# Performance work log

Measured on AMD Instinct MI355X. Metric: run time of the kernel, lower is better.

## Reference

```python
import jax, jax.numpy as jnp
import numpy as np

B = 131072
IN_DIM = 310   # 300 + zdimension_Gap(10)
H1 = 128       # g_neural_network_width
D = 100        # hard-coded data_t / generate_data width
SLOPE = 0.01   # torch LeakyReLU default negative_slope


def _leaky(v):
    return jnp.where(v >= 0, v, SLOPE * v)


def setup_inputs() -> dict:
    key = jax.random.key(0)
    ks = jax.random.split(key, 8)
    # kaiming_normal fan_in, a=0: std = sqrt(2 / fan_in)
    W1 = jax.random.normal(ks[0], (IN_DIM, 10), jnp.float32) * np.sqrt(2.0 / IN_DIM)
    b1 = jnp.zeros((10,), jnp.float32)
    W2 = jax.random.normal(ks[1], (10, H1), jnp.float32) * np.sqrt(2.0 / 10)
    b2 = jnp.zeros((H1,), jnp.float32)
    W3 = jax.random.normal(ks[2], (H1, 2), jnp.float32) * np.sqrt(2.0 / H1)
    b3 = jnp.zeros((2,), jnp.float32)
    x = jax.random.normal(ks[3], (B, IN_DIM), jnp.float32)
    data_t = jax.random.normal(ks[4], (B, D), jnp.float32)
    return {"x": x, "data_t": data_t, "W1": W1, "b1": b1,
            "W2": W2, "b2": b2, "W3": W3, "b3": b3}


def reference(x, data_t, W1, b1, W2, b2, W3, b3):
    # 3-layer MLP with LeakyReLU -> coeff [B, 2]
    h = _leaky(x @ W1 + b1)
    h = _leaky(h @ W2 + b2)
    coeff = _leaky(h @ W3 + b3)
    # polynomial basis: only power-1 (data_t) and power-2 (data_t**2) terms are used
    t2 = data_t * data_t  # [B, D]
    # generate_data[i] = coeff[i,0]*data_t[i] + coeff[i,1]*data_t[i]**2 (vectorized over batch)
    generate_data = coeff[:, 0:1] * data_t + coeff[:, 1:2] * t2
    return generate_data
```

## Files before the change

kernel.cpp:

```cpp
#include <hip/hip_runtime.h>
#include <stdint.h>

typedef float f32x2 __attribute__((ext_vector_type(2)));
typedef float f32x4 __attribute__((ext_vector_type(4)));

#define TILE_F 19840
#define NTPB   4
#define PSTR   82
#define CP_OFF 5248
#define CPSTR  18
#define A_F    8192
#define APW    1024
#define BPW    1456
#define LDSF   (TILE_F + 128)
#define LDS_BYTES (LDSF * 4)

__device__ __forceinline__ float leaky(float v) { return fmaxf(v, 0.01f * v); }
__device__ __forceinline__ f32x2 leaky2(f32x2 v) {
    return __builtin_elementwise_max(v, v * 0.01f);
}

__device__ __forceinline__ void gload16(const float* g, float* l) {
    auto gp = reinterpret_cast<const float __attribute__((address_space(1)))*>(
        reinterpret_cast<uintptr_t>(g));
    auto lp = reinterpret_cast<float __attribute__((address_space(3)))*>(
        reinterpret_cast<uintptr_t>(l));
    __builtin_amdgcn_global_load_lds(gp, lp, 16, 0, 0);
}

__device__ __forceinline__ void stage_B(const float* src, float* dst, int lane) {
    #pragma unroll
    for (int i = 0; i < 5; ++i) gload16(src + i * 256, dst + i * 256);
    if (lane < 44) gload16(src + 5 * 256, dst + 5 * 256);
}
__device__ __forceinline__ void stage_A(const float* src, float* dst) {
    #pragma unroll
    for (int i = 0; i < 4; ++i) gload16(src + i * 256, dst + i * 256);
}

template<int KQ>
__device__ __forceinline__ void fma_xk(const float* xk, const float* __restrict__ Wb,
                                       float* acc) {
    #pragma unroll
    for (int k = 0; k < KQ; ++k) {
        #pragma unroll
        for (int j = 0; j < 10; ++j)
            acc[j] = fmaf(xk[k], Wb[k * 10 + j], acc[j]);
    }
}

__global__ __launch_bounds__(512, 4) void gen_mlp_r14(
    const float* __restrict__ x, const float* __restrict__ data_t,
    const float* __restrict__ W1, const float* __restrict__ b1,
    const float* __restrict__ W2, const float* __restrict__ b2,
    const float* __restrict__ W3, const float* __restrict__ b3,
    float* __restrict__ out)
{
    extern __shared__ float lds[];
    float* buf = lds;
    float* ccs = lds + TILE_F;

    const int t    = threadIdx.x;
    const int lane = t & 63;
    const int row  = lane;
    const int wq   = __builtin_amdgcn_readfirstlane(t >> 6);

    const int tile0 = blockIdx.x * NTPB;

    {
        const float* g = x + (size_t)tile0 * TILE_F;
        stage_A(g + wq * APW + lane * 4,       buf + wq * APW);
        stage_B(g + A_F + wq * BPW + lane * 4, buf + A_F + wq * BPW, lane);
    }
    asm volatile("s_waitcnt vmcnt(0)" ::: "memory");
    __builtin_amdgcn_s_barrier();

    #pragma unroll 1
    for (int it = 0; it < NTPB; ++it) {
        const int tile  = tile0 + it;
        const int tnext = (it + 1 < NTPB) ? tile + 1 : tile0;
        const float* gnext = x + (size_t)tnext * TILE_F;

        const f32x4* dt4 = (const f32x4*)data_t + (size_t)tile * 1600;
        f32x4 tv0 = dt4[t], tv1 = dt4[512 + t], tv2 = dt4[1024 + t], tv3;
        if (t < 64) tv3 = dt4[1536 + t];

        float xk[40];
        {
            const float* xr = buf + row * 310 + wq * 40;
            if (wq == 7) {
                #pragma unroll
                for (int q = 0; q < 15; ++q)
                    *(f32x2*)&xk[2 * q] = *(const f32x2*)(xr + 2 * q);
            } else {
                #pragma unroll
                for (int q = 0; q < 20; ++q)
                    *(f32x2*)&xk[2 * q] = *(const f32x2*)(xr + 2 * q);
            }
        }
        asm volatile("s_waitcnt lgkmcnt(0)" ::: "memory");
        __builtin_amdgcn_s_barrier();

        stage_B(gnext + A_F + wq * BPW + lane * 4, buf + A_F + wq * BPW, lane);

        float acc[10] = {0,0,0,0,0,0,0,0,0,0};
        if (wq == 7) fma_xk<30>(xk, W1 + 2800, acc);
        else         fma_xk<40>(xk, W1 + wq * 400, acc);

        {
            float* pw = buf + row * PSTR + wq * 10;
            #pragma unroll
            for (int j = 0; j < 5; ++j)
                *(f32x2*)(pw + 2 * j) = (f32x2){acc[2 * j], acc[2 * j + 1]};
        }
        asm volatile("s_waitcnt lgkmcnt(0)" ::: "memory");
        __builtin_amdgcn_s_barrier();

        float h1[10];
        {
            const float* pr = buf + row * PSTR;
            float s[10];
            #pragma unroll
            for (int j = 0; j < 10; ++j) s[j] = b1[j];
            #pragma unroll
            for (int sl = 0; sl < 8; ++sl) {
                #pragma unroll
                for (int m = 0; m < 5; ++m) {
                    f32x2 v = *(const f32x2*)(pr + sl * 10 + 2 * m);
                    s[2 * m]     += v.x;
                    s[2 * m + 1] += v.y;
                }
            }
            #pragma unroll
            for (int j = 0; j < 10; ++j) h1[j] = leaky(s[j]);
        }

        float hh[16];
        #pragma unroll
        for (int jj = 0; jj < 16; ++jj) hh[jj] = b2[wq * 16 + jj];
        #pragma unroll
        for (int k = 0; k < 10; ++k) {
            #pragma unroll
            for (int jj = 0; jj < 16; ++jj)
                hh[jj] = fmaf(h1[k], W2[k * 128 + wq * 16 + jj], hh[jj]);
        }
        f32x2 p = {0.f, 0.f};
        #pragma unroll
        for (int jj = 0; jj < 16; ++jj) {
            const float s = leaky(hh[jj]);
            p.x = fmaf(s, W3[(wq * 16 + jj) * 2 + 0], p.x);
            p.y = fmaf(s, W3[(wq * 16 + jj) * 2 + 1], p.y);
        }

        *(f32x2*)(buf + CP_OFF + row * CPSTR + 2 * wq) = p;
        asm volatile("s_waitcnt lgkmcnt(0)" ::: "memory");
        __builtin_amdgcn_s_barrier();

        if (wq == 0) {
            const float* cb = buf + CP_OFF + row * CPSTR;
            f32x2 q = {b3[0], b3[1]};
            #pragma unroll
            for (int i = 0; i < 8; ++i) {
                f32x2 v = *(const f32x2*)(cb + 2 * i);
                q.x += v.x;
                q.y += v.y;
            }
            *(f32x2*)(ccs + 2 * row) = leaky2(q);
        }
        asm volatile("s_waitcnt lgkmcnt(0)" ::: "memory");
        __builtin_amdgcn_s_barrier();

        stage_A(gnext + wq * APW + lane * 4, buf + wq * APW);

        f32x4* o4 = (f32x4*)out + (size_t)tile * 1600;
        {
            f32x2 cc = *(const f32x2*)(ccs + 2 * (t / 25));
            o4[t] = tv0 * (tv0 * cc.y + cc.x);
        }
        {
            const int idx = 512 + t;
            f32x2 cc = *(const f32x2*)(ccs + 2 * (idx / 25));
            o4[idx] = tv1 * (tv1 * cc.y + cc.x);
        }
        {
            const int idx = 1024 + t;
            f32x2 cc = *(const f32x2*)(ccs + 2 * (idx / 25));
            o4[idx] = tv2 * (tv2 * cc.y + cc.x);
        }
        if (t < 64) {
            const int idx = 1536 + t;
            f32x2 cc = *(const f32x2*)(ccs + 2 * (idx / 25));
            o4[idx] = tv3 * (tv3 * cc.y + cc.x);
        }

        asm volatile("s_waitcnt vmcnt(3)" ::: "memory");
        __builtin_amdgcn_s_barrier();
    }
}

extern "C" void kernel_launch(void* const* d_in, const int* in_sizes, int n_in,
                              void* d_out, int out_size, void* d_ws, size_t ws_size,
                              hipStream_t stream) {
    const float* x      = (const float*)d_in[0];
    const float* data_t = (const float*)d_in[1];
    const float* W1     = (const float*)d_in[2];
    const float* b1     = (const float*)d_in[3];
    const float* W2     = (const float*)d_in[4];
    const float* b2     = (const float*)d_in[5];
    const float* W3     = (const float*)d_in[6];
    const float* b3     = (const float*)d_in[7];
    float* out = (float*)d_out;

    hipFuncSetAttribute((const void*)gen_mlp_r14,
                        hipFuncAttributeMaxDynamicSharedMemorySize, LDS_BYTES);
    gen_mlp_r14<<<512, 512, LDS_BYTES, stream>>>(x, data_t, W1, b1, W2, b2, W3, b3, out);
}
```

Before: 60.32 us.

## Double block to 1024 threads, splitting K across 16 waves with pairwise reduction

Each block now runs 16 waves instead of 8. The 310-wide first-layer dot product is split into 20-column slices per wave, and the layer-2 and layer-3 work is split into 8 hidden units per wave. An extra LDS reduction step folds the 16 partial sums down to 8 before the existing reduce, and the LDS staging offsets and the global-to-LDS copy partition are recomputed to match. The aim is more latency hiding and shorter per-thread serial FMA chains, at the cost of one extra barrier per tile and possibly lower occupancy per CU.

```diff
diff --git a/kernel.cpp b/kernel.cpp
--- a/kernel.cpp
+++ b/kernel.cpp
@@ -6,12 +6,12 @@
 
 #define TILE_F 19840
 #define NTPB   4
-#define PSTR   82
-#define CP_OFF 5248
-#define CPSTR  18
-#define A_F    8192
-#define APW    1024
-#define BPW    1456
+#define PSTR   162
+#define CP_OFF 10368
+#define CPSTR  34
+#define A_F    12544
+#define APW    784
+#define BPW    456
 #define LDSF   (TILE_F + 128)
 #define LDS_BYTES (LDSF * 4)
 
@@ -28,14 +28,14 @@
     __builtin_amdgcn_global_load_lds(gp, lp, 16, 0, 0);
 }
 
+__device__ __forceinline__ void stage_A(const float* src, float* dst, int lane) {
+    #pragma unroll
+    for (int i = 0; i < 3; ++i) gload16(src + i * 256, dst + i * 256);
+    if (lane < 4) gload16(src + 768, dst + 768);
+}
 __device__ __forceinline__ void stage_B(const float* src, float* dst, int lane) {
-    #pragma unroll
-    for (int i = 0; i < 5; ++i) gload16(src + i * 256, dst + i * 256);
-    if (lane < 44) gload16(src + 5 * 256, dst + 5 * 256);
-}
-__device__ __forceinline__ void stage_A(const float* src, float* dst) {
-    #pragma unroll
-    for (int i = 0; i < 4; ++i) gload16(src + i * 256, dst + i * 256);
+    gload16(src, dst);
+    if (lane < 50) gload16(src + 256, dst + 256);
 }
 
 template<int KQ>
@@ -49,7 +49,7 @@
     }
 }
 
-__global__ __launch_bounds__(512, 4) void gen_mlp_r14(
+__global__ __launch_bounds__(1024, 8) void gen_mlp_r17(
     const float* __restrict__ x, const float* __restrict__ data_t,
     const float* __restrict__ W1, const float* __restrict__ b1,
     const float* __restrict__ W2, const float* __restrict__ b2,
@@ -69,7 +69,7 @@
 
     {
         const float* g = x + (size_t)tile0 * TILE_F;
-        stage_A(g + wq * APW + lane * 4,       buf + wq * APW);
+        stage_A(g + wq * APW + lane * 4,       buf + wq * APW,       lane);
         stage_B(g + A_F + wq * BPW + lane * 4, buf + A_F + wq * BPW, lane);
     }
     asm volatile("s_waitcnt vmcnt(0)" ::: "memory");
@@ -82,19 +82,19 @@
         const float* gnext = x + (size_t)tnext * TILE_F;
 
         const f32x4* dt4 = (const f32x4*)data_t + (size_t)tile * 1600;
-        f32x4 tv0 = dt4[t], tv1 = dt4[512 + t], tv2 = dt4[1024 + t], tv3;
-        if (t < 64) tv3 = dt4[1536 + t];
-
-        float xk[40];
-        {
-            const float* xr = buf + row * 310 + wq * 40;
-            if (wq == 7) {
+        f32x4 tv0 = dt4[t], tv1;
+        if (t < 576) tv1 = dt4[1024 + t];
+
+        float xk[20];
+        {
+            const float* xr = buf + row * 310 + wq * 20;
+            if (wq == 15) {
                 #pragma unroll
-                for (int q = 0; q < 15; ++q)
+                for (int q = 0; q < 5; ++q)
                     *(f32x2*)&xk[2 * q] = *(const f32x2*)(xr + 2 * q);
             } else {
                 #pragma unroll
-                for (int q = 0; q < 20; ++q)
+                for (int q = 0; q < 10; ++q)
                     *(f32x2*)&xk[2 * q] = *(const f32x2*)(xr + 2 * q);
             }
         }
@@ -104,14 +104,26 @@
         stage_B(gnext + A_F + wq * BPW + lane * 4, buf + A_F + wq * BPW, lane);
 
         float acc[10] = {0,0,0,0,0,0,0,0,0,0};
-        if (wq == 7) fma_xk<30>(xk, W1 + 2800, acc);
-        else         fma_xk<40>(xk, W1 + wq * 400, acc);
+        if (wq == 15) fma_xk<10>(xk, W1 + 3000, acc);
+        else          fma_xk<20>(xk, W1 + wq * 200, acc);
 
         {
             float* pw = buf + row * PSTR + wq * 10;
             #pragma unroll
             for (int j = 0; j < 5; ++j)
                 *(f32x2*)(pw + 2 * j) = (f32x2){acc[2 * j], acc[2 * j + 1]};
+        }
+        asm volatile("s_waitcnt lgkmcnt(0)" ::: "memory");
+        __builtin_amdgcn_s_barrier();
+
+        if (wq < 8) {
+            float* pr = buf + row * PSTR + wq * 10;
+            const float* ph = buf + row * PSTR + (wq + 8) * 10;
+            #pragma unroll
+            for (int m = 0; m < 5; ++m) {
+                f32x2 v = *(const f32x2*)(pr + 2 * m) + *(const f32x2*)(ph + 2 * m);
+                *(f32x2*)(pr + 2 * m) = v;
+            }
         }
         asm volatile("s_waitcnt lgkmcnt(0)" ::: "memory");
         __builtin_amdgcn_s_barrier();
@@ -135,21 +147,21 @@
             for (int j = 0; j < 10; ++j) h1[j] = leaky(s[j]);
         }
 
-        float hh[16];
-        #pragma unroll
-        for (int jj = 0; jj < 16; ++jj) hh[jj] = b2[wq * 16 + jj];
+        float hh[8];
+        #pragma unroll
+        for (int jj = 0; jj < 8; ++jj) hh[jj] = b2[wq * 8 + jj];
         #pragma unroll
         for (int k = 0; k < 10; ++k) {
             #pragma unroll
-            for (int jj = 0; jj < 16; ++jj)
-                hh[jj] = fmaf(h1[k], W2[k * 128 + wq * 16 + jj], hh[jj]);
+            for (int jj = 0; jj < 8; ++jj)
+                hh[jj] = fmaf(h1[k], W2[k * 128 + wq * 8 + jj], hh[jj]);
         }
         f32x2 p = {0.f, 0.f};
         #pragma unroll
-        for (int jj = 0; jj < 16; ++jj) {
+        for (int jj = 0; jj < 8; ++jj) {
             const float s = leaky(hh[jj]);
-            p.x = fmaf(s, W3[(wq * 16 + jj) * 2 + 0], p.x);
-            p.y = fmaf(s, W3[(wq * 16 + jj) * 2 + 1], p.y);
+            p.x = fmaf(s, W3[(wq * 8 + jj) * 2 + 0], p.x);
+            p.y = fmaf(s, W3[(wq * 8 + jj) * 2 + 1], p.y);
         }
 
         *(f32x2*)(buf + CP_OFF + row * CPSTR + 2 * wq) = p;
@@ -160,7 +172,7 @@
             const float* cb = buf + CP_OFF + row * CPSTR;
             f32x2 q = {b3[0], b3[1]};
             #pragma unroll
-            for (int i = 0; i < 8; ++i) {
+            for (int i = 0; i < 16; ++i) {
                 f32x2 v = *(const f32x2*)(cb + 2 * i);
                 q.x += v.x;
                 q.y += v.y;
@@ -170,30 +182,20 @@
         asm volatile("s_waitcnt lgkmcnt(0)" ::: "memory");
         __builtin_amdgcn_s_barrier();
 
-        stage_A(gnext + wq * APW + lane * 4, buf + wq * APW);
+        stage_A(gnext + wq * APW + lane * 4, buf + wq * APW, lane);
 
         f32x4* o4 = (f32x4*)out + (size_t)tile * 1600;
         {
             f32x2 cc = *(const f32x2*)(ccs + 2 * (t / 25));
             o4[t] = tv0 * (tv0 * cc.y + cc.x);
         }
-        {
-            const int idx = 512 + t;
+        if (t < 576) {
+            const int idx = 1024 + t;
             f32x2 cc = *(const f32x2*)(ccs + 2 * (idx / 25));
             o4[idx] = tv1 * (tv1 * cc.y + cc.x);
         }
-        {
-            const int idx = 1024 + t;
-            f32x2 cc = *(const f32x2*)(ccs + 2 * (idx / 25));
-            o4[idx] = tv2 * (tv2 * cc.y + cc.x);
-        }
-        if (t < 64) {
-            const int idx = 1536 + t;
-            f32x2 cc = *(const f32x2*)(ccs + 2 * (idx / 25));
-            o4[idx] = tv3 * (tv3 * cc.y + cc.x);
-        }
-
-        asm volatile("s_waitcnt vmcnt(3)" ::: "memory");
+
+        asm volatile("s_waitcnt vmcnt(1)" ::: "memory");
         __builtin_amdgcn_s_barrier();
     }
 }
@@ -211,7 +213,7 @@
     const float* b3     = (const float*)d_in[7];
     float* out = (float*)d_out;
 
-    hipFuncSetAttribute((const void*)gen_mlp_r14,
+    hipFuncSetAttribute((const void*)gen_mlp_r17,
                         hipFuncAttributeMaxDynamicSharedMemorySize, LDS_BYTES);
-    gen_mlp_r14<<<512, 512, LDS_BYTES, stream>>>(x, data_t, W1, b1, W2, b2, W3, b3, out);
-}
+    gen_mlp_r17<<<512, 1024, LDS_BYTES, stream>>>(x, data_t, W1, b1, W2, b2, W3, b3, out);
+}
```

Measured after the change: 56.43 us. 6.5% less time.
